# Performance work log

Measured on AMD Instinct MI355X. Metric: run time of the kernel, lower is better.

## Reference

```python
import jax, jax.numpy as jnp
import numpy as np

# ---- static config (mirrors GaussianLSS __init__) ----
ORF_H, ORF_W = 256, 704
FC, FH, FW = 128, 32, 88
D_ST, D_END, D_STEP = 4.0, 45.0, 1.0
OUT_C = 128
ERROR_TOL = 1.0
OPACITY_THR = 0.05
XB = (-50.0, 50.0, 1.0)
YB = (-50.0, 50.0, 1.0)
BEV_H = int(round((YB[1] - YB[0]) / YB[2]))
BEV_W = int(round((XB[1] - XB[0]) / XB[2]))
DS = np.arange(D_ST, D_END, D_STEP, dtype=np.float32)
D = DS.shape[0]  # 41
BN_EPS = 1e-3
CHUNK = 512      # gaussians composited per scan step (16896 = 33*512)
B, NCAM = 1, 6


def make_frustum():
    ds = jnp.broadcast_to(jnp.asarray(DS)[:, None, None], (D, FH, FW))
    xs = jnp.broadcast_to(jnp.linspace(0.0, ORF_W - 1.0, FW)[None, None, :], (D, FH, FW))
    ys = jnp.broadcast_to(jnp.linspace(0.0, ORF_H - 1.0, FH)[None, :, None], (D, FH, FW))
    return jnp.stack([xs, ys, ds], -1)  # [D,FH,FW,3]


def get_geometry(rots, trans, intrins, post_rots, post_trans):
    fr = make_frustum()
    pts = fr[None, None] - post_trans[:, :, None, None, None, :]
    pts = jnp.einsum('bnij,bndhwj->bndhwi', jnp.linalg.inv(post_rots), pts)
    pts = jnp.concatenate([pts[..., :2] * pts[..., 2:3], pts[..., 2:3]], -1)
    comb = jnp.einsum('bnij,bnjk->bnik', rots, jnp.linalg.inv(intrins))
    pts = jnp.einsum('bnij,bndhwj->bndhwi', comb, pts) + trans[:, :, None, None, None, :]
    return pts  # [B,N,D,FH,FW,3] ego-frame frustum points


def conv2d(x, w, b, pad):
    y = jax.lax.conv_general_dilated(x, w, (1, 1), [(pad, pad), (pad, pad)],
                                     dimension_numbers=('NCHW', 'OIHW', 'NCHW'))
    return y + b[None, :, None, None]


def bnorm(x, g, bt, m, v):
    s = (g / jnp.sqrt(v + BN_EPS))[None, :, None, None]
    return (x - m[None, :, None, None]) * s + bt[None, :, None, None]


def splat(means, cov6, colors, ops, valid_in):
    # Differentiable BEV gaussian rasterization (3DGS math, orthographic BEV camera,
    # all depths equal -> compositing in stable gaussian-index order).
    H, W = BEV_H, BEV_W
    sh, sw = H / 2.0, W / 2.0  # h/h_meters with FoV=2 (BEVCamera)
    my = -sh * means[:, 1] + H / 2.0  # pixel row (full_proj_transform row 0)
    mx = -sw * means[:, 0] + W / 2.0  # pixel col (row 1)
    a = sh * sh * cov6[:, 3] + 0.3    # 2D cov = J Sigma_xy J^T, +0.3 low-pass as in 3DGS
    c = sw * sw * cov6[:, 0] + 0.3
    b = sh * sw * cov6[:, 1]
    det = a * c - b * b
    valid = valid_in & (det > 0)
    inv_det = jnp.where(det > 0, 1.0 / det, 0.0)
    cA, cB, cC = c * inv_det, -b * inv_det, a * inv_det
    pi = jnp.repeat(jnp.arange(H, dtype=jnp.float32), W)  # [P] pixel rows
    pj = jnp.tile(jnp.arange(W, dtype=jnp.float32), H)    # [P] pixel cols
    G = means.shape[0]
    nchunk = G // CHUNK
    resh = lambda x: x.reshape((nchunk, CHUNK) + x.shape[1:])
    chunks = (resh(my), resh(mx), resh(cA), resh(cB), resh(cC),
              resh(ops), resh(valid), resh(colors))

    def body(carry, ch):
        logT, acc = carry
        my_c, mx_c, A, Bc, Cc, op_c, val_c, col_c = ch
        dI = pi[None, :] - my_c[:, None]                     # [Gc,P]
        dJ = pj[None, :] - mx_c[:, None]
        q = A[:, None] * dI * dI + 2.0 * Bc[:, None] * dI * dJ + Cc[:, None] * dJ * dJ
        alpha = jnp.minimum(0.99, op_c[:, None] * jnp.exp(-0.5 * q))
        alpha = jnp.where(val_c[:, None] & (q >= 0) & (alpha >= 1.0 / 255.0), alpha, 0.0)
        log1m = jnp.log1p(-alpha)
        cum = jnp.cumsum(log1m, axis=0)
        T = jnp.exp(logT[None, :] + cum - log1m)             # transmittance before each gaussian
        acc = acc + jnp.einsum('gp,gc->pc', alpha * T, col_c)
        return (logT + cum[-1], acc), None

    P = H * W
    init = (jnp.zeros((P,), jnp.float32), jnp.zeros((P, colors.shape[1]), jnp.float32))
    (_, acc), _ = jax.lax.scan(jax.checkpoint(body), init, chunks)
    return acc.reshape(H, W, -1).transpose(2, 0, 1)  # [C,H,W], bg is zeros


def _forward(cam2ego_rot, cam2ego_trans, cam_intrins, post_cam2ego_rot, post_cam2ego_trans,
             img_feats, conv1_w, conv1_b, bn1_g, bn1_b, bn1_m, bn1_v,
             conv2_w, conv2_b, bn2_g, bn2_b, bn2_m, bn2_v, conv3_w, conv3_b):
    geom = get_geometry(cam2ego_rot, cam2ego_trans, cam_intrins, post_cam2ego_rot, post_cam2ego_trans)
    b, n = img_feats.shape[:2]
    x = img_feats.reshape(b * n, FC, FH, FW)
    x = jax.nn.relu(bnorm(conv2d(x, conv1_w, conv1_b, 1), bn1_g, bn1_b, bn1_m, bn1_v))
    x = jax.nn.relu(bnorm(conv2d(x, conv2_w, conv2_b, 1), bn2_g, bn2_b, bn2_m, bn2_v))
    x = conv2d(x, conv3_w, conv3_b, 0)
    depth_prob = jax.nn.softmax(x[:, :D], axis=1).reshape(b, n, D, FH, FW)
    opac = jax.nn.sigmoid(x[:, D:D + 1]).reshape(b, n, FH, FW)
    feats = x[:, D + 1:].reshape(b, n, OUT_C, FH, FW)
    # per-pixel gaussian moments of the depth distribution (compute_gaussian)
    means = jnp.einsum('bndhw,bndhwi->bnhwi', depth_prob, geom)
    delta = means[:, :, None] - geom                                       # [B,N,D,FH,FW,3]
    cov = jnp.einsum('bndhw,bndhwi,bndhwj->bnhwij', depth_prob, delta, delta) * (ERROR_TOL ** 2 / 9.0)
    center = jnp.array([(XB[0] + XB[1]) / 2.0, (YB[0] + YB[1]) / 2.0, 0.0], jnp.float32)
    scale = jnp.array([2.0 / (XB[1] - XB[0]), 2.0 / (YB[1] - YB[0]), 1.0], jnp.float32)
    m_n = (means - center) * scale
    cov_n = cov * (scale[:, None] * scale[None, :])
    cov6 = jnp.stack([cov_n[..., 0, 0], cov_n[..., 0, 1], cov_n[..., 0, 2],
                      cov_n[..., 1, 1], cov_n[..., 1, 2], cov_n[..., 2, 2]], -1)
    g = n * FH * FW
    colors = feats.transpose(0, 1, 3, 4, 2).reshape(b, g, OUT_C)
    m_n = m_n.reshape(b, g, 3)
    cov6 = cov6.reshape(b, g, 6)
    ops = opac.reshape(b, g)
    mask = ops > OPACITY_THR  # opacity filtering == zero contribution, order preserved
    bev = jax.vmap(splat)(m_n, cov6, colors, ops, mask)                    # [B,C,H,W]
    num_gaussians = mask.astype(jnp.float32).sum(-1).mean()
    return bev, num_gaussians


def setup_inputs():
    key = jax.random.key(0)
    ks = jax.random.split(key, 8)
    # camera-to-ego rotations: cam->ego axis permutation composed with per-camera yaw
    yaw = np.linspace(0.0, 2.0 * np.pi, NCAM, endpoint=False).astype(np.float32)
    cz, sz = np.cos(yaw), np.sin(yaw)
    rotz = np.zeros((NCAM, 3, 3), np.float32)
    rotz[:, 0, 0] = cz; rotz[:, 0, 1] = -sz
    rotz[:, 1, 0] = sz; rotz[:, 1, 1] = cz
    rotz[:, 2, 2] = 1.0
    perm = np.array([[0.0, 0.0, 1.0], [-1.0, 0.0, 0.0], [0.0, -1.0, 0.0]], np.float32)
    rots = np.einsum('nij,jk->nik', rotz, perm)
    cam2ego_rot = jnp.asarray(np.broadcast_to(rots, (B, NCAM, 3, 3)).copy())
    cam2ego_trans = jax.random.normal(ks[0], (B, NCAM, 3), jnp.float32)
    K = np.array([[600.0, 0.0, ORF_W / 2.0], [0.0, 600.0, ORF_H / 2.0], [0.0, 0.0, 1.0]], np.float32)
    cam_intrins = jnp.asarray(np.broadcast_to(K, (B, NCAM, 3, 3)).copy())
    post_cam2ego_rot = jnp.broadcast_to(jnp.eye(3, dtype=jnp.float32), (B, NCAM, 3, 3)) + jnp.zeros((B, NCAM, 3, 3), jnp.float32)
    post_cam2ego_trans = jnp.zeros((B, NCAM, 3), jnp.float32)
    img_feats = jax.random.normal(ks[1], (B, NCAM, FC, FH, FW), jnp.float32)
    def conv_init(k, o, i, kh, kw):
        return jax.random.normal(k, (o, i, kh, kw), jnp.float32) * (1.0 / np.sqrt(i * kh * kw))
    return dict(cam2ego_rot=cam2ego_rot, cam2ego_trans=cam2ego_trans, cam_intrins=cam_intrins,
                post_cam2ego_rot=post_cam2ego_rot, post_cam2ego_trans=post_cam2ego_trans,
                img_feats=img_feats,
                conv1_w=conv_init(ks[2], FC, FC, 3, 3), conv1_b=jnp.zeros((FC,), jnp.float32),
                bn1_g=jnp.ones((FC,), jnp.float32), bn1_b=jnp.zeros((FC,), jnp.float32),
                bn1_m=jnp.zeros((FC,), jnp.float32), bn1_v=jnp.ones((FC,), jnp.float32),
                conv2_w=conv_init(ks[3], FC, FC, 3, 3), conv2_b=jnp.zeros((FC,), jnp.float32),
                bn2_g=jnp.ones((FC,), jnp.float32), bn2_b=jnp.zeros((FC,), jnp.float32),
                bn2_m=jnp.zeros((FC,), jnp.float32), bn2_v=jnp.ones((FC,), jnp.float32),
                conv3_w=conv_init(ks[4], OUT_C + D + 1, FC, 1, 1),
                conv3_b=jax.random.normal(ks[5], (OUT_C + D + 1,), jnp.float32) * 0.1)


def reference(cam2ego_rot, cam2ego_trans, cam_intrins, post_cam2ego_rot, post_cam2ego_trans,
              img_feats, conv1_w, conv1_b, bn1_g, bn1_b, bn1_m, bn1_v,
              conv2_w, conv2_b, bn2_g, bn2_b, bn2_m, bn2_v, conv3_w, conv3_b):
    return _forward(cam2ego_rot, cam2ego_trans, cam_intrins, post_cam2ego_rot, post_cam2ego_trans,
                    img_feats, conv1_w, conv1_b, bn1_g, bn1_b, bn1_m, bn1_v,
                    conv2_w, conv2_b, bn2_g, bn2_b, bn2_m, bn2_v, conv3_w, conv3_b)
```

## Files before the change

### kernel.cpp

```cpp
#include <hip/hip_runtime.h>

#define NCAM 6
#define FC   128
#define FH_  32
#define FW_  88
#define NPIX (FH_*FW_)
#define PH   34
#define PW   92
#define PPIX (PH*PW)
#define ND   41
#define X3D  42
#define OUTC 128
#define GTOT (NCAM*NPIX)
#define BEVH 100
#define BEVW 100
#define NPXB (BEVH*BEVW)
#define NTILE 25
#define NWORD 264
#define WCAP  70000
#define CSIZE 64
#define CBLK  2048

#define SZA     (NCAM*FC*PPIX)
#define WS_CAM  0
// ... 5 lines not shown
#define WS_BASE (WS_WL + WCAP)

__device__ inline void inv3x3(const float* m, float* o) {
    float a=m[0],b=m[1],c=m[2],d=m[3],e=m[4],f=m[5],g=m[6],h=m[7],i=m[8];
    float A=e*i-f*h, B=c*h-b*i, C=b*f-c*e;
    float Dd=f*g-d*i, E=a*i-c*g, F=c*d-a*f;
    float Gg=d*h-e*g, H=b*g-a*h, I=a*e-b*d;
    float r = 1.0f/(a*A + b*Dd + c*Gg);
    o[0]=A*r; o[1]=B*r; o[2]=C*r; o[3]=Dd*r; o[4]=E*r; o[5]=F*r;
    o[6]=Gg*r; o[7]=H*r; o[8]=I*r;
}

__global__ void cam_consts_kernel(const float* __restrict__ rot, const float* __restrict__ tr,
                                  const float* __restrict__ intr, const float* __restrict__ prot,
                                  const float* __restrict__ ptr_, float* __restrict__ cam) {
    int n = threadIdx.x;
    if (n >= NCAM) return;
    float M1[9], Ki[9];
    inv3x3(prot + n*9, M1);
    inv3x3(intr + n*9, Ki);
    const float* R = rot + n*9;
    float* c = cam + n*24;
    for (int i=0;i<9;i++) c[i] = M1[i];
    for (int i=0;i<3;i++) c[9+i] = ptr_[n*3+i];
    for (int i=0;i<3;i++)
        for (int j=0;j<3;j++)
            c[12+i*3+j] = R[i*3+0]*Ki[0+j] + R[i*3+1]*Ki[3+j] + R[i*3+2]*Ki[6+j];
    for (int i=0;i<3;i++) c[21+i] = tr[n*3+i];
}

__global__ __launch_bounds__(256) void pad_input_kernel(const float* __restrict__ src,
                                                        float* __restrict__ dst) {
    int idx = blockIdx.x*256 + threadIdx.x;
    int plane = idx / NPIX, px = idx - plane*NPIX;
    int y = px / FW_, x = px - y*FW_;
    dst[(size_t)plane*PPIX + (y+1)*PW + (x+1)] = src[idx];
}

__global__ __launch_bounds__(256) void conv3x3_pf_kernel(
        const float* __restrict__ in, float* __restrict__ out, const float* __restrict__ w,
        const float* __restrict__ cb, const float* __restrict__ bg, const float* __restrict__ bb,
        const float* __restrict__ bm, const float* __restrict__ bv) {
    const int n   = blockIdx.x;
    const int co0 = blockIdx.y * 4;
    const int qid = blockIdx.z * 256 + threadIdx.x;
    if (qid >= 704) return;
    const int y = qid / 22, x0 = (qid - y*22) * 4;
    float scale[4], shift[4];
    #pragma unroll
    for (int c=0;c<4;c++) {
        float s = bg[co0+c] * rsqrtf(bv[co0+c] + 1e-3f);
        scale[c] = s;
        shift[c] = (cb[co0+c] - bm[co0+c]) * s + bb[co0+c];
    }
    float acc[4][4] = {};
    const float* ip = in + (size_t)n*FC*PPIX + y*PW + x0;
    const float* wb = w + (size_t)co0*FC*9;
    float4 p4[3]; float2 p2[3];
    #pragma unroll
    for (int r=0;r<3;r++) {
        p4[r] = *(const float4*)(ip + r*PW);
        p2[r] = *(const float2*)(ip + r*PW + 4);
    }
    for (int ci=0; ci<FC; ++ci) {
        float v[3][6];
        #pragma unroll
        for (int r=0;r<3;r++) {
            v[r][0]=p4[r].x; v[r][1]=p4[r].y; v[r][2]=p4[r].z; v[r][3]=p4[r].w;
            v[r][4]=p2[r].x; v[r][5]=p2[r].y;
        }
        if (ci + 1 < FC) {
            const float* ipn = ip + PPIX;
            #pragma unroll
            for (int r=0;r<3;r++) {
                p4[r] = *(const float4*)(ipn + r*PW);
                p2[r] = *(const float2*)(ipn + r*PW + 4);
            }
        }
// ... 41 lines not shown
    }
    const float* ip = in + (size_t)n*FC*PPIX + pp;
    #pragma unroll 4
    for (int ci=0; ci<FC; ++ci) {
        float v = ip[(size_t)ci*PPIX];
        #pragma unroll
        for (int k=0;k<8;k++) acc[k] = fmaf(wr[k][ci], v, acc[k]);
    }
    #pragma unroll
    for (int k=0;k<8;k++) {
        int co = co0 + k;
        if (co < X3D)
            x3d[((size_t)n*X3D + co)*NPIX + px] = acc[k];
        else if (co < 170)
            colors[(((size_t)(n*NPIX + px)) << 7) + (co - X3D)] = acc[k];
    }
}

__global__ __launch_bounds__(256) void moments_kernel(const float* __restrict__ x3,
        const float* __restrict__ cam, float* __restrict__ gauss, float* __restrict__ ng) {
    int gi = blockIdx.x*256 + threadIdx.x;
    int n  = gi / NPIX;
    int p  = gi - n*NPIX;
    int h  = p / FW_, xp = p - h*FW_;
    const float* cc = cam + n*24;
    float u = xp * (703.0f/87.0f);
    float v = h  * (255.0f/31.0f);
    float fx = u - cc[9], fy = v - cc[10], fz = -cc[11];
    float p0x = cc[0]*fx + cc[1]*fy + cc[2]*fz;
    float p0y = cc[3]*fx + cc[4]*fy + cc[5]*fz;
    float p0z = cc[6]*fx + cc[7]*fy + cc[8]*fz;
    const float* lg = x3 + (size_t)n*X3D*NPIX + p;

    float mxl = -1e30f;
    for (int d=0; d<ND; ++d) mxl = fmaxf(mxl, lg[(size_t)d*NPIX]);
    float s=0.f, sgx=0.f, sgy=0.f;
    for (int d=0; d<ND; ++d) {
        float e  = __expf(lg[(size_t)d*NPIX] - mxl);
        float dz = 4.0f + (float)d;
        float pz = p0z + dz*cc[8];
        float px = (p0x + dz*cc[2]) * pz;
        float py = (p0y + dz*cc[5]) * pz;
        float gx = cc[12]*px + cc[13]*py + cc[14]*pz + cc[21];
        float gy = cc[15]*px + cc[16]*py + cc[17]*pz + cc[22];
        s += e; sgx += e*gx; sgy += e*gy;
    }
    float inv_s = 1.0f/s;
    float mex = sgx*inv_s, mey = sgy*inv_s;
    float cxx=0.f, cxy=0.f, cyy=0.f;
    for (int d=0; d<ND; ++d) {
        float e  = __expf(lg[(size_t)d*NPIX] - mxl);
        float dz = 4.0f + (float)d;
        float pz = p0z + dz*cc[8];
        float px = (p0x + dz*cc[2]) * pz;
        float py = (p0y + dz*cc[5]) * pz;
        float gx = cc[12]*px + cc[13]*py + cc[14]*pz + cc[21];
        float gy = cc[15]*px + cc[16]*py + cc[17]*pz + cc[22];
        float dxv = gx - mex, dyv = gy - mey;
        cxx += e*dxv*dxv; cxy += e*dxv*dyv; cyy += e*dyv*dyv;
    }
    const float k9 = inv_s * (1.0f/9.0f);
    cxx *= k9; cxy *= k9; cyy *= k9;

    float lo = lg[(size_t)ND*NPIX];
    float op = 1.0f/(1.0f + __expf(-lo));
    bool mask = op > 0.05f;

    const float SC = 0.02f, SH = 50.0f, SW = 50.0f;
    float my = -SH*(mey*SC) + 50.0f;
    float mx = -SW*(mex*SC) + 50.0f;
    float a  = SH*SH*(cyy*SC*SC) + 0.3f;
    float b  = SH*SW*(cxy*SC*SC);
    float c  = SW*SW*(cxx*SC*SC) + 0.3f;
    float det = a*c - b*b;
    bool valid = mask && (det > 0.0f);
    float A, B2, C, qm, ri, rj;
    if (valid) {
        float idet = 1.0f/det;
        A = c*idet; B2 = -2.0f*b*idet; C = a*idet;
        qm = 2.0f*__logf(255.0f*op);
        ri = sqrtf(qm*a); rj = sqrtf(qm*c);
    } else { A=B2=C=0.f; qm=-1.0f; ri=-1e30f; rj=-1e30f; }
    float* gp = gauss + (size_t)gi*8;
    gp[0]=my; gp[1]=mx; gp[2]=A; gp[3]=B2; gp[4]=C; gp[5]=qm; gp[6]=ri; gp[7]=rj;
// ... 81 lines not shown
        unsigned short* __restrict__ list, int* __restrict__ wl) {
    __shared__ unsigned long long sw[NWORD];
    __shared__ int wpre[NWORD];
    const int tile = blockIdx.x, t = threadIdx.x;
    if (t < NWORD) sw[t] = masks[(size_t)tile*NWORD + t];
    __syncthreads();
    if (t == 0) {
        int run = 0;
        for (int w2 = 0; w2 < NWORD; ++w2) { wpre[w2] = run; run += __popcll(sw[w2]); }
    }
    __syncthreads();
    if (t < NWORD) {
        unsigned long long m = sw[t];
        int pos = off[tile] + wpre[t], base = t << 6;
        while (m) { int b = __builtin_ctzll(m); m &= m - 1; list[pos++] = (unsigned short)(base + b); }
    }
    int nch = (cnt[tile] + CSIZE-1)/CSIZE;
    int c0 = choff[tile];
    if (t < nch && c0 + t < WCAP) wl[c0 + t] = (tile << 9) | t;
}

__device__ inline float eval_alpha(const float4 g0, const float4 g1, float fi, float fj) {
    float dI = fi - g0.x, dJ = fj - g0.y;
    float q = dI*(g0.z*dI + g0.w*dJ) + g1.x*dJ*dJ;
    if (q < 0.0f || q > g1.y) return 0.0f;
    return fminf(0.99f, 0.003921568627f * __expf(0.5f*(g1.y - q)));
}

__global__ __launch_bounds__(256) void chunk_sums_kernel(const float* __restrict__ gauss,
        const unsigned short* __restrict__ list, const int* __restrict__ cnt,
        const int* __restrict__ off, const int* __restrict__ wl, const int* __restrict__ nwork,
        float* __restrict__ base) {
    const int nw = nwork[0];
    const int t = threadIdx.x;
    const int px = t & 15, kg = t >> 4;
    __shared__ unsigned short slist[CSIZE];
    __shared__ float red[16][17];
    for (int e = blockIdx.x; e < nw; e += gridDim.x) {
        int v = wl[e], tile = v >> 9, c = v & 511;
        int hbase = off[tile] + (c << 6);
        int nh = min(CSIZE, cnt[tile] - (c << 6));
        if (t < nh) slist[t] = list[hbase + t];
        __syncthreads();
        const int i0 = (tile / NTILE) * 4, j0 = (tile % NTILE) * 4;
        const float fi = (float)(i0 + (px >> 2)), fj = (float)(j0 + (px & 3));
        float s = 0.0f;
        for (int k = kg; k < nh; k += 16) {
            int g = slist[k];
            float4 g0 = *(const float4*)(gauss + ((size_t)g << 3));
            float4 g1 = *(const float4*)(gauss + ((size_t)g << 3) + 4);
            float a = eval_alpha(g0, g1, fi, fj);
            if (a > 0.0f) s += __logf(1.0f - a);
        }
        red[kg][px] = s;
        __syncthreads();
        if (t < 16) {
            float acc = 0.0f;
            #pragma unroll
            for (int k2 = 0; k2 < 16; ++k2) acc += red[k2][t];
            base[(size_t)e*16 + t] = acc;
        }
        __syncthreads();
    }
}

__global__ __launch_bounds__(256) void chunk_prefix_kernel(const int* __restrict__ choff,
                                                           float* __restrict__ base) {
    __shared__ float part[16][17];
    const int tile = blockIdx.x, t = threadIdx.x;
    const int c0 = choff[tile], nch = choff[tile+1] - c0;
    if (nch == 0) return;
    const int px = t & 15, cg = t >> 4;
    const int L16 = (nch + 15) >> 4;
    const int a0 = cg*L16, a1 = min(nch, a0 + L16);
    float s = 0.0f;
    for (int c = a0; c < a1; ++c) s += base[(size_t)(c0 + c)*16 + px];
    part[cg][px] = s;
    __syncthreads();
    if (t < 16) {
        float run = 0.0f;
        #pragma unroll
        for (int k = 0; k < 16; ++k) { float tmp = part[k][t]; part[k][t] = run; run += tmp; }
    }
    __syncthreads();
    float run = part[cg][px];
    for (int c = a0; c < a1; ++c) {
        size_t idx = (size_t)(c0 + c)*16 + px;
        float tmp = base[idx];
        base[idx] = run;
        run += tmp;
    }
}

__global__ __launch_bounds__(256) void composite_kernel(const float* __restrict__ gauss,
        const float* __restrict__ colors, const unsigned short* __restrict__ list,
        const int* __restrict__ cnt, const int* __restrict__ off, const int* __restrict__ wl,
        const int* __restrict__ nwork, const float* __restrict__ base, float* __restrict__ out) {
    const int nw = nwork[0];
    const int t = threadIdx.x;
    const int lane = t & 63;
    const int e_px = t >> 4, e_kg = t & 15;
    const int a_cs4 = t & 31, a_pxq = t >> 5;
    __shared__ unsigned short slist[2][CSIZE];
    __shared__ float s_w[CSIZE][17];
    const int per = (nw + CBLK - 1) / CBLK;
    int e0 = blockIdx.x * per;
    if (e0 >= nw) return;
    int e1 = min(nw, e0 + per);

    float4 acc0 = make_float4(0.f,0.f,0.f,0.f);
    float4 acc1 = make_float4(0.f,0.f,0.f,0.f);
    int cur_tile = wl[e0] >> 9;
    int cur_i0 = (cur_tile / NTILE) * 4, cur_j0 = (cur_tile % NTILE) * 4;

    int buf = 0;
    {
        int v = wl[e0], tl = v >> 9, c = v & 511;
        int nh0 = min(CSIZE, cnt[tl] - (c << 6));
        if (t < nh0) slist[0][t] = list[off[tl] + (c << 6) + t];
    }

    for (int e = e0; e < e1; ++e) {
        int v = wl[e], tile = v >> 9, c = v & 511;
        if (tile != cur_tile) {
            const int pix0 = (cur_i0 + (a_pxq >> 2)) * BEVW + cur_j0 + (a_pxq & 3);
            const int pix1 = pix0 + 2 * BEVW;
            float* op = out + (size_t)(a_cs4 << 2) * NPXB;
            atomicAdd(op + 0*NPXB + pix0, acc0.x); atomicAdd(op + 1*NPXB + pix0, acc0.y);
            atomicAdd(op + 2*NPXB + pix0, acc0.z); atomicAdd(op + 3*NPXB + pix0, acc0.w);
            atomicAdd(op + 0*NPXB + pix1, acc1.x); atomicAdd(op + 1*NPXB + pix1, acc1.y);
            atomicAdd(op + 2*NPXB + pix1, acc1.z); atomicAdd(op + 3*NPXB + pix1, acc1.w);
            acc0 = make_float4(0.f,0.f,0.f,0.f);
            acc1 = make_float4(0.f,0.f,0.f,0.f);
            cur_tile = tile;
            cur_i0 = (tile / NTILE) * 4; cur_j0 = (tile % NTILE) * 4;
        }
        const int nh = min(CSIZE, cnt[cur_tile] - (c << 6));
        __syncthreads();
        if (e + 1 < e1) {
            int v2 = wl[e+1], tl2 = v2 >> 9, c2 = v2 & 511;
            int nh2 = min(CSIZE, cnt[tl2] - (c2 << 6));
            if (t < nh2) slist[buf^1][t] = list[off[tl2] + (c2 << 6) + t];
        }
        {
            const float fi = (float)(cur_i0 + (e_px >> 2)), fj = (float)(cur_j0 + (e_px & 3));
            const int k0 = e_kg << 2;
            float a4[4]; float lsum = 0.0f;
            #pragma unroll
            for (int i = 0; i < 4; ++i) {
                int k = k0 + i;
                float a = 0.0f;
                if (k < nh) {
                    int g = slist[buf][k];
                    float4 g0 = *(const float4*)(gauss + ((size_t)g << 3));
                    float4 g1 = *(const float4*)(gauss + ((size_t)g << 3) + 4);
                    a = eval_alpha(g0, g1, fi, fj);
                }
                a4[i] = a;
                if (a > 0.0f) lsum += __logf(1.0f - a);
            }
            float s = lsum;
            #pragma unroll
            for (int o = 1; o < 16; o <<= 1) {
                float u = __shfl_up(s, (unsigned)o, 64);
                if ((lane & 15) >= o) s += u;
            }
            float T = __expf(base[(size_t)e*16 + e_px] + (s - lsum));
            #pragma unroll
            for (int i = 0; i < 4; ++i) {
                float wv = a4[i] * T; T -= wv;
                s_w[k0 + i][e_px] = wv;
            }
        }
        __syncthreads();
        const float* colbase = colors;
        if (nh == CSIZE) {
            #pragma unroll 8
            for (int k = 0; k < CSIZE; ++k) {
                int g = slist[buf][k];
                float w0 = s_w[k][a_pxq];
                float w1 = s_w[k][a_pxq + 8];
                float4 cl = *(const float4*)(colbase + ((size_t)g << 7) + (a_cs4 << 2));
                acc0.x = fmaf(w0, cl.x, acc0.x); acc0.y = fmaf(w0, cl.y, acc0.y);
                acc0.z = fmaf(w0, cl.z, acc0.z); acc0.w = fmaf(w0, cl.w, acc0.w);
                acc1.x = fmaf(w1, cl.x, acc1.x); acc1.y = fmaf(w1, cl.y, acc1.y);
                acc1.z = fmaf(w1, cl.z, acc1.z); acc1.w = fmaf(w1, cl.w, acc1.w);
            }
        } else {
            #pragma unroll 4
            for (int k = 0; k < nh; ++k) {
                int g = slist[buf][k];
                float w0 = s_w[k][a_pxq];
                float w1 = s_w[k][a_pxq + 8];
                float4 cl = *(const float4*)(colbase + ((size_t)g << 7) + (a_cs4 << 2));
                acc0.x = fmaf(w0, cl.x, acc0.x); acc0.y = fmaf(w0, cl.y, acc0.y);
                acc0.z = fmaf(w0, cl.z, acc0.z); acc0.w = fmaf(w0, cl.w, acc0.w);
                acc1.x = fmaf(w1, cl.x, acc1.x); acc1.y = fmaf(w1, cl.y, acc1.y);
                acc1.z = fmaf(w1, cl.z, acc1.z); acc1.w = fmaf(w1, cl.w, acc1.w);
            }
        }
        buf ^= 1;
    }
    const int pix0 = (cur_i0 + (a_pxq >> 2)) * BEVW + cur_j0 + (a_pxq & 3);
    const int pix1 = pix0 + 2 * BEVW;
    float* op = out + (size_t)(a_cs4 << 2) * NPXB;
    atomicAdd(op + 0*NPXB + pix0, acc0.x); atomicAdd(op + 1*NPXB + pix0, acc0.y);
    atomicAdd(op + 2*NPXB + pix0, acc0.z); atomicAdd(op + 3*NPXB + pix0, acc0.w);
    atomicAdd(op + 0*NPXB + pix1, acc1.x); atomicAdd(op + 1*NPXB + pix1, acc1.y);
    atomicAdd(op + 2*NPXB + pix1, acc1.z); atomicAdd(op + 3*NPXB + pix1, acc1.w);
}

extern "C" void kernel_launch(void* const* d_in, const int* in_sizes, int n_in,
                              void* d_out, int out_size, void* d_ws, size_t ws_size,
                              hipStream_t stream) {
    const float* rot  = (const float*)d_in[0];
    const float* tr   = (const float*)d_in[1];
    const float* intr = (const float*)d_in[2];
    const float* prot = (const float*)d_in[3];
    const float* ptr_ = (const float*)d_in[4];
    const float* img  = (const float*)d_in[5];
    const float* c1w  = (const float*)d_in[6];  const float* c1b = (const float*)d_in[7];
    const float* b1g  = (const float*)d_in[8];  const float* b1b = (const float*)d_in[9];
    const float* b1m  = (const float*)d_in[10]; const float* b1v = (const float*)d_in[11];
    const float* c2w  = (const float*)d_in[12]; const float* c2b = (const float*)d_in[13];
    const float* b2g  = (const float*)d_in[14]; const float* b2b = (const float*)d_in[15];
    const float* b2m  = (const float*)d_in[16]; const float* b2v = (const float*)d_in[17];
    const float* c3w  = (const float*)d_in[18]; const float* c3b = (const float*)d_in[19];
    float* out = (float*)d_out;
    float* ws  = (float*)d_ws;
    float* CAM = ws + WS_CAM;
    float* RA  = ws + WS_A;
    float* RB  = ws + WS_RB;
    float* X3B = ws + WS_X3;
    float* GS  = ws + WS_GS;
    int*   WL  = (int*)(ws + WS_WL);
    float* BASE = ws + WS_BASE;
    unsigned long long* MASKS = (unsigned long long*)X3B;
    int* AUXI = (int*)(ws + WS_X3 + 330000);
    int* CNT = AUXI;
    int* OFF = AUXI + 640;
    int* CHOFF = AUXI + 1280;
    int* NWORK = AUXI + 1920;
    unsigned short* LIST = (unsigned short*)RA;
    float* COL = RB;
    float* ngp = out + (size_t)NPXB*OUTC;

    cam_consts_kernel<<<1, 64, 0, stream>>>(rot, tr, intr, prot, ptr_, CAM);
    (void)hipMemsetAsync(RA, 0, (size_t)SZA*sizeof(float), stream);
    (void)hipMemsetAsync(RB, 0, (size_t)SZA*sizeof(float), stream);
    pad_input_kernel<<<NCAM*FC*NPIX/256, 256, 0, stream>>>(img, RA);
    conv3x3_pf_kernel<<<dim3(NCAM,32,3), 256, 0, stream>>>(RA, RB, c1w, c1b, b1g, b1b, b1m, b1v);
    conv3x3_pf_kernel<<<dim3(NCAM,32,3), 256, 0, stream>>>(RB, RA, c2w, c2b, b2g, b2b, b2m, b2v);
    conv1x1_kernel<<<dim3(NCAM,11,22), 256, 0, stream>>>(RA, X3B, COL, c3w, c3b);
    (void)hipMemsetAsync(ngp, 0, sizeof(float), stream);
    (void)hipMemsetAsync(out, 0, (size_t)NPXB*OUTC*sizeof(float), stream);
    moments_kernel<<<GTOT/256, 256, 0, stream>>>(X3B, CAM, GS, ngp);
    (void)hipMemsetAsync(MASKS, 0, (size_t)NTILE*NTILE*NWORD*sizeof(unsigned long long), stream);
    build_masks_kernel<<<GTOT/256, 256, 0, stream>>>(GS, MASKS);
    cnt_kernel<<<NTILE*NTILE, 256, 0, stream>>>(MASKS, CNT);
    scan_kernel<<<1, 640, 0, stream>>>(CNT, OFF, CHOFF, NWORK);
    fill_kernel<<<NTILE*NTILE, 256, 0, stream>>>(MASKS, CNT, OFF, CHOFF, LIST, WL);
    chunk_sums_kernel<<<8192, 256, 0, stream>>>(GS, LIST, CNT, OFF, WL, NWORK, BASE);
    chunk_prefix_kernel<<<NTILE*NTILE, 256, 0, stream>>>(CHOFF, BASE);
    composite_kernel<<<CBLK, 256, 0, stream>>>(GS, COL, LIST, CNT, OFF, WL, NWORK, BASE, out);
}
```

Before: 487.4 us.

## Pipeline composite weights, wave-level chunk sums, cache logits, fuse padding memset

The composite kernel now computes transmittance weights for the next chunk while accumulating colors for the current one. It triple-buffers the gaussian index lists and double-buffers the weights, which removes one barrier per chunk. chunk_sums becomes one wavefront per work item that reduces with shuffles instead of shared memory and block barriers. moments caches the 41 logits and their exponentials in registers instead of reloading and recomputing them, and pad_input writes the zero border itself so one memset goes away. The trade-off is more shared memory and register pressure, which may lower occupancy.

```diff
diff --git a/kernel.cpp b/kernel.cpp
--- a/kernel.cpp
+++ b/kernel.cpp
@@ -61,9 +61,13 @@
 __global__ __launch_bounds__(256) void pad_input_kernel(const float* __restrict__ src,
                                                         float* __restrict__ dst) {
     int idx = blockIdx.x*256 + threadIdx.x;
-    int plane = idx / NPIX, px = idx - plane*NPIX;
-    int y = px / FW_, x = px - y*FW_;
-    dst[(size_t)plane*PPIX + (y+1)*PW + (x+1)] = src[idx];
+    if (idx >= NCAM*FC*PPIX) return;
+    int plane = idx / PPIX, pp = idx - plane*PPIX;
+    int y = pp / PW, x = pp - y*PW;
+    float v = 0.0f;
+    if (y >= 1 && y <= FH_ && x >= 1 && x <= FW_)
+        v = src[(size_t)plane*NPIX + (y-1)*FW_ + (x-1)];
+    dst[idx] = v;
 }
 
 __global__ __launch_bounds__(256) void conv3x3_pf_kernel(
@@ -180,11 +184,19 @@
     float p0z = cc[6]*fx + cc[7]*fy + cc[8]*fz;
     const float* lg = x3 + (size_t)n*X3D*NPIX + p;
 
+    float lgv[ND];
+    #pragma unroll
+    for (int d=0; d<ND; ++d) lgv[d] = lg[(size_t)d*NPIX];
+
     float mxl = -1e30f;
-    for (int d=0; d<ND; ++d) mxl = fmaxf(mxl, lg[(size_t)d*NPIX]);
+    #pragma unroll
+    for (int d=0; d<ND; ++d) mxl = fmaxf(mxl, lgv[d]);
+
     float s=0.f, sgx=0.f, sgy=0.f;
+    #pragma unroll
     for (int d=0; d<ND; ++d) {
-        float e  = __expf(lg[(size_t)d*NPIX] - mxl);
+        float e  = __expf(lgv[d] - mxl);
+        lgv[d] = e;
         float dz = 4.0f + (float)d;
         float pz = p0z + dz*cc[8];
         float px = (p0x + dz*cc[2]) * pz;
@@ -196,8 +208,9 @@
     float inv_s = 1.0f/s;
     float mex = sgx*inv_s, mey = sgy*inv_s;
     float cxx=0.f, cxy=0.f, cyy=0.f;
+    #pragma unroll
     for (int d=0; d<ND; ++d) {
-        float e  = __expf(lg[(size_t)d*NPIX] - mxl);
+        float e  = lgv[d];
         float dz = 4.0f + (float)d;
         float pz = p0z + dz*cc[8];
         float px = (p0x + dz*cc[2]) * pz;
@@ -345,35 +358,27 @@
         const int* __restrict__ off, const int* __restrict__ wl, const int* __restrict__ nwork,
         float* __restrict__ base) {
     const int nw = nwork[0];
-    const int t = threadIdx.x;
-    const int px = t & 15, kg = t >> 4;
-    __shared__ unsigned short slist[CSIZE];
-    __shared__ float red[16][17];
-    for (int e = blockIdx.x; e < nw; e += gridDim.x) {
+    const int lane = threadIdx.x & 63;
+    const int wid  = (blockIdx.x * 256 + threadIdx.x) >> 6;
+    const int nwv  = (gridDim.x * 256) >> 6;
+    const int px = lane & 15, kg = lane >> 4;
+    for (int e = wid; e < nw; e += nwv) {
         int v = wl[e], tile = v >> 9, c = v & 511;
         int hbase = off[tile] + (c << 6);
         int nh = min(CSIZE, cnt[tile] - (c << 6));
-        if (t < nh) slist[t] = list[hbase + t];
-        __syncthreads();
         const int i0 = (tile / NTILE) * 4, j0 = (tile % NTILE) * 4;
         const float fi = (float)(i0 + (px >> 2)), fj = (float)(j0 + (px & 3));
         float s = 0.0f;
-        for (int k = kg; k < nh; k += 16) {
-            int g = slist[k];
+        for (int k = kg; k < nh; k += 4) {
+            int g = list[hbase + k];
             float4 g0 = *(const float4*)(gauss + ((size_t)g << 3));
             float4 g1 = *(const float4*)(gauss + ((size_t)g << 3) + 4);
             float a = eval_alpha(g0, g1, fi, fj);
             if (a > 0.0f) s += __logf(1.0f - a);
         }
-        red[kg][px] = s;
-        __syncthreads();
-        if (t < 16) {
-            float acc = 0.0f;
-            #pragma unroll
-            for (int k2 = 0; k2 < 16; ++k2) acc += red[k2][t];
-            base[(size_t)e*16 + t] = acc;
-        }
-        __syncthreads();
+        s += __shfl_xor(s, 16, 64);
+        s += __shfl_xor(s, 32, 64);
+        if (lane < 16) base[(size_t)e*16 + lane] = s;
     }
 }
 
@@ -414,8 +419,8 @@
     const int lane = t & 63;
     const int e_px = t >> 4, e_kg = t & 15;
     const int a_cs4 = t & 31, a_pxq = t >> 5;
-    __shared__ unsigned short slist[2][CSIZE];
-    __shared__ float s_w[CSIZE][17];
+    __shared__ unsigned short slist[3][CSIZE];
+    __shared__ float s_w[2][CSIZE][17];
     const int per = (nw + CBLK - 1) / CBLK;
     int e0 = blockIdx.x * per;
     if (e0 >= nw) return;
@@ -426,45 +431,70 @@
     int cur_tile = wl[e0] >> 9;
     int cur_i0 = (cur_tile / NTILE) * 4, cur_j0 = (cur_tile % NTILE) * 4;
 
-    int buf = 0;
     {
         int v = wl[e0], tl = v >> 9, c = v & 511;
         int nh0 = min(CSIZE, cnt[tl] - (c << 6));
-        if (t < nh0) slist[0][t] = list[off[tl] + (c << 6) + t];
+        if (t < nh0) slist[e0 % 3][t] = list[off[tl] + (c << 6) + t];
+        if (e0 + 1 < e1) {
+            int v2 = wl[e0+1], tl2 = v2 >> 9, c2 = v2 & 511;
+            int nh2 = min(CSIZE, cnt[tl2] - (c2 << 6));
+            if (t < nh2) slist[(e0+1) % 3][t] = list[off[tl2] + (c2 << 6) + t];
+        }
+    }
+    __syncthreads();
+    {
+        int v = wl[e0], tl = v >> 9, c = v & 511;
+        int nh_e = min(CSIZE, cnt[tl] - (c << 6));
+        const float fi = (float)(cur_i0 + (e_px >> 2)), fj = (float)(cur_j0 + (e_px & 3));
+        const int k0 = e_kg << 2;
+        float a4[4]; float lsum = 0.0f;
+        #pragma unroll
+        for (int i = 0; i < 4; ++i) {
+            int k = k0 + i;
+            float a = 0.0f;
+            if (k < nh_e) {
+                int g = slist[e0 % 3][k];
+                float4 g0 = *(const float4*)(gauss + ((size_t)g << 3));
+                float4 g1 = *(const float4*)(gauss + ((size_t)g << 3) + 4);
+                a = eval_alpha(g0, g1, fi, fj);
+            }
+            a4[i] = a;
+            if (a > 0.0f) lsum += __logf(1.0f - a);
+        }
+        float s = lsum;
+        #pragma unroll
+        for (int o = 1; o < 16; o <<= 1) {
+            float u = __shfl_up(s, (unsigned)o, 64);
+            if ((lane & 15) >= o) s += u;
+        }
+        float T = __expf(base[(size_t)e0*16 + e_px] + (s - lsum));
+        #pragma unroll
+        for (int i = 0; i < 4; ++i) {
+            float wv = a4[i] * T; T -= wv;
+            s_w[e0 & 1][k0 + i][e_px] = wv;
+        }
     }
 
     for (int e = e0; e < e1; ++e) {
-        int v = wl[e], tile = v >> 9, c = v & 511;
-        if (tile != cur_tile) {
-            const int pix0 = (cur_i0 + (a_pxq >> 2)) * BEVW + cur_j0 + (a_pxq & 3);
-            const int pix1 = pix0 + 2 * BEVW;
-            float* op = out + (size_t)(a_cs4 << 2) * NPXB;
-            atomicAdd(op + 0*NPXB + pix0, acc0.x); atomicAdd(op + 1*NPXB + pix0, acc0.y);
-            atomicAdd(op + 2*NPXB + pix0, acc0.z); atomicAdd(op + 3*NPXB + pix0, acc0.w);
-            atomicAdd(op + 0*NPXB + pix1, acc1.x); atomicAdd(op + 1*NPXB + pix1, acc1.y);
-            atomicAdd(op + 2*NPXB + pix1, acc1.z); atomicAdd(op + 3*NPXB + pix1, acc1.w);
-            acc0 = make_float4(0.f,0.f,0.f,0.f);
-            acc1 = make_float4(0.f,0.f,0.f,0.f);
-            cur_tile = tile;
-            cur_i0 = (tile / NTILE) * 4; cur_j0 = (tile % NTILE) * 4;
-        }
-        const int nh = min(CSIZE, cnt[cur_tile] - (c << 6));
         __syncthreads();
+        if (e + 2 < e1) {
+            int v2 = wl[e+2], tl2 = v2 >> 9, c2 = v2 & 511;
+            int nh2 = min(CSIZE, cnt[tl2] - (c2 << 6));
+            if (t < nh2) slist[(e+2) % 3][t] = list[off[tl2] + (c2 << 6) + t];
+        }
         if (e + 1 < e1) {
-            int v2 = wl[e+1], tl2 = v2 >> 9, c2 = v2 & 511;
-            int nh2 = min(CSIZE, cnt[tl2] - (c2 << 6));
-            if (t < nh2) slist[buf^1][t] = list[off[tl2] + (c2 << 6) + t];
-        }
-        {
-            const float fi = (float)(cur_i0 + (e_px >> 2)), fj = (float)(cur_j0 + (e_px & 3));
+            int v = wl[e+1], tl = v >> 9, c = v & 511;
+            int nh_e = min(CSIZE, cnt[tl] - (c << 6));
+            const int ii0 = (tl / NTILE) * 4, jj0 = (tl % NTILE) * 4;
+            const float fi = (float)(ii0 + (e_px >> 2)), fj = (float)(jj0 + (e_px & 3));
             const int k0 = e_kg << 2;
             float a4[4]; float lsum = 0.0f;
             #pragma unroll
             for (int i = 0; i < 4; ++i) {
                 int k = k0 + i;
                 float a = 0.0f;
-                if (k < nh) {
-                    int g = slist[buf][k];
+                if (k < nh_e) {
+                    int g = slist[(e+1) % 3][k];
                     float4 g0 = *(const float4*)(gauss + ((size_t)g << 3));
                     float4 g1 = *(const float4*)(gauss + ((size_t)g << 3) + 4);
                     a = eval_alpha(g0, g1, fi, fj);
@@ -478,41 +508,57 @@
                 float u = __shfl_up(s, (unsigned)o, 64);
                 if ((lane & 15) >= o) s += u;
             }
-            float T = __expf(base[(size_t)e*16 + e_px] + (s - lsum));
+            float T = __expf(base[(size_t)(e+1)*16 + e_px] + (s - lsum));
             #pragma unroll
             for (int i = 0; i < 4; ++i) {
                 float wv = a4[i] * T; T -= wv;
-                s_w[k0 + i][e_px] = wv;
-            }
-        }
-        __syncthreads();
-        const float* colbase = colors;
-        if (nh == CSIZE) {
-            #pragma unroll 8
-            for (int k = 0; k < CSIZE; ++k) {
-                int g = slist[buf][k];
-                float w0 = s_w[k][a_pxq];
-                float w1 = s_w[k][a_pxq + 8];
-                float4 cl = *(const float4*)(colbase + ((size_t)g << 7) + (a_cs4 << 2));
-                acc0.x = fmaf(w0, cl.x, acc0.x); acc0.y = fmaf(w0, cl.y, acc0.y);
-                acc0.z = fmaf(w0, cl.z, acc0.z); acc0.w = fmaf(w0, cl.w, acc0.w);
-                acc1.x = fmaf(w1, cl.x, acc1.x); acc1.y = fmaf(w1, cl.y, acc1.y);
-                acc1.z = fmaf(w1, cl.z, acc1.z); acc1.w = fmaf(w1, cl.w, acc1.w);
-            }
-        } else {
-            #pragma unroll 4
-            for (int k = 0; k < nh; ++k) {
-                int g = slist[buf][k];
-                float w0 = s_w[k][a_pxq];
-                float w1 = s_w[k][a_pxq + 8];
-                float4 cl = *(const float4*)(colbase + ((size_t)g << 7) + (a_cs4 << 2));
-                acc0.x = fmaf(w0, cl.x, acc0.x); acc0.y = fmaf(w0, cl.y, acc0.y);
-                acc0.z = fmaf(w0, cl.z, acc0.z); acc0.w = fmaf(w0, cl.w, acc0.w);
-                acc1.x = fmaf(w1, cl.x, acc1.x); acc1.y = fmaf(w1, cl.y, acc1.y);
-                acc1.z = fmaf(w1, cl.z, acc1.z); acc1.w = fmaf(w1, cl.w, acc1.w);
-            }
-        }
-        buf ^= 1;
+                s_w[(e+1) & 1][k0 + i][e_px] = wv;
+            }
+        }
+        {
+            int v = wl[e], tile = v >> 9, c = v & 511;
+            if (tile != cur_tile) {
+                const int pix0 = (cur_i0 + (a_pxq >> 2)) * BEVW + cur_j0 + (a_pxq & 3);
+                const int pix1 = pix0 + 2 * BEVW;
+                float* op = out + (size_t)(a_cs4 << 2) * NPXB;
+                atomicAdd(op + 0*NPXB + pix0, acc0.x); atomicAdd(op + 1*NPXB + pix0, acc0.y);
+                atomicAdd(op + 2*NPXB + pix0, acc0.z); atomicAdd(op + 3*NPXB + pix0, acc0.w);
+                atomicAdd(op + 0*NPXB + pix1, acc1.x); atomicAdd(op + 1*NPXB + pix1, acc1.y);
+                atomicAdd(op + 2*NPXB + pix1, acc1.z); atomicAdd(op + 3*NPXB + pix1, acc1.w);
+                acc0 = make_float4(0.f,0.f,0.f,0.f);
+                acc1 = make_float4(0.f,0.f,0.f,0.f);
+                cur_tile = tile;
+                cur_i0 = (tile / NTILE) * 4; cur_j0 = (tile % NTILE) * 4;
+            }
+            const int nh = min(CSIZE, cnt[tile] - (c << 6));
+            const float (*swp)[17] = s_w[e & 1];
+            const unsigned short* slp = slist[e % 3];
+            if (nh == CSIZE) {
+                #pragma unroll 8
+                for (int k = 0; k < CSIZE; ++k) {
+                    int g = slp[k];
+                    float w0 = swp[k][a_pxq];
+                    float w1 = swp[k][a_pxq + 8];
+                    float4 cl = *(const float4*)(colors + ((size_t)g << 7) + (a_cs4 << 2));
+                    acc0.x = fmaf(w0, cl.x, acc0.x); acc0.y = fmaf(w0, cl.y, acc0.y);
+                    acc0.z = fmaf(w0, cl.z, acc0.z); acc0.w = fmaf(w0, cl.w, acc0.w);
+                    acc1.x = fmaf(w1, cl.x, acc1.x); acc1.y = fmaf(w1, cl.y, acc1.y);
+                    acc1.z = fmaf(w1, cl.z, acc1.z); acc1.w = fmaf(w1, cl.w, acc1.w);
+                }
+            } else {
+                #pragma unroll 4
+                for (int k = 0; k < nh; ++k) {
+                    int g = slp[k];
+                    float w0 = swp[k][a_pxq];
+                    float w1 = swp[k][a_pxq + 8];
+                    float4 cl = *(const float4*)(colors + ((size_t)g << 7) + (a_cs4 << 2));
+                    acc0.x = fmaf(w0, cl.x, acc0.x); acc0.y = fmaf(w0, cl.y, acc0.y);
+                    acc0.z = fmaf(w0, cl.z, acc0.z); acc0.w = fmaf(w0, cl.w, acc0.w);
+                    acc1.x = fmaf(w1, cl.x, acc1.x); acc1.y = fmaf(w1, cl.y, acc1.y);
+                    acc1.z = fmaf(w1, cl.z, acc1.z); acc1.w = fmaf(w1, cl.w, acc1.w);
+                }
+            }
+        }
     }
     const int pix0 = (cur_i0 + (a_pxq >> 2)) * BEVW + cur_j0 + (a_pxq & 3);
     const int pix1 = pix0 + 2 * BEVW;
@@ -559,9 +605,8 @@
     float* ngp = out + (size_t)NPXB*OUTC;
 
     cam_consts_kernel<<<1, 64, 0, stream>>>(rot, tr, intr, prot, ptr_, CAM);
-    (void)hipMemsetAsync(RA, 0, (size_t)SZA*sizeof(float), stream);
     (void)hipMemsetAsync(RB, 0, (size_t)SZA*sizeof(float), stream);
-    pad_input_kernel<<<NCAM*FC*NPIX/256, 256, 0, stream>>>(img, RA);
+    pad_input_kernel<<<(NCAM*FC*PPIX + 255)/256, 256, 0, stream>>>(img, RA);
     conv3x3_pf_kernel<<<dim3(NCAM,32,3), 256, 0, stream>>>(RA, RB, c1w, c1b, b1g, b1b, b1m, b1v);
     conv3x3_pf_kernel<<<dim3(NCAM,32,3), 256, 0, stream>>>(RB, RA, c2w, c2b, b2g, b2b, b2m, b2v);
     conv1x1_kernel<<<dim3(NCAM,11,22), 256, 0, stream>>>(RA, X3B, COL, c3w, c3b);
```

New measurement: 476.5 us. -2.3%, faster.

## Replace log-sum transmittance with products, fuse padding, retile conv and composite

Applied to the files above, without the earlier changes.

The pad kernel now writes the whole padded buffer, zeros included, so one memset goes away. The conv3x3 launch drops to 128-thread blocks with twice the z-blocks. The moments kernel caches the logits and exp values in registers instead of reloading them and recomputing exp. The transmittance sums switch from log/exp to direct products, and chunk_sums becomes one wavefront per work item with shuffle reductions, which avoids shared memory and barriers. The composite kernel remaps threads so each one holds 4 pixels × 4 channels and splits the gaussians across two halves. Products may underflow and lose some precision compared with log sums.

```diff
diff --git a/kernel.cpp b/kernel.cpp
--- a/kernel.cpp
+++ b/kernel.cpp
@@ -61,18 +61,22 @@
 __global__ __launch_bounds__(256) void pad_input_kernel(const float* __restrict__ src,
                                                         float* __restrict__ dst) {
     int idx = blockIdx.x*256 + threadIdx.x;
-    int plane = idx / NPIX, px = idx - plane*NPIX;
-    int y = px / FW_, x = px - y*FW_;
-    dst[(size_t)plane*PPIX + (y+1)*PW + (x+1)] = src[idx];
-}
-
-__global__ __launch_bounds__(256) void conv3x3_pf_kernel(
+    if (idx >= NCAM*FC*PPIX) return;
+    int plane = idx / PPIX, pp = idx - plane*PPIX;
+    int y = pp / PW, x = pp - y*PW;
+    float v = 0.0f;
+    if (y >= 1 && y <= FH_ && x >= 1 && x <= FW_)
+        v = src[(size_t)plane*NPIX + (y-1)*FW_ + (x-1)];
+    dst[idx] = v;
+}
+
+__global__ __launch_bounds__(128) void conv3x3_pf_kernel(
         const float* __restrict__ in, float* __restrict__ out, const float* __restrict__ w,
         const float* __restrict__ cb, const float* __restrict__ bg, const float* __restrict__ bb,
         const float* __restrict__ bm, const float* __restrict__ bv) {
     const int n   = blockIdx.x;
     const int co0 = blockIdx.y * 4;
-    const int qid = blockIdx.z * 256 + threadIdx.x;
+    const int qid = blockIdx.z * 128 + threadIdx.x;
     if (qid >= 704) return;
     const int y = qid / 22, x0 = (qid - y*22) * 4;
     float scale[4], shift[4];
@@ -180,11 +184,19 @@
     float p0z = cc[6]*fx + cc[7]*fy + cc[8]*fz;
     const float* lg = x3 + (size_t)n*X3D*NPIX + p;
 
+    float lgv[ND];
+    #pragma unroll
+    for (int d=0; d<ND; ++d) lgv[d] = lg[(size_t)d*NPIX];
+
     float mxl = -1e30f;
-    for (int d=0; d<ND; ++d) mxl = fmaxf(mxl, lg[(size_t)d*NPIX]);
+    #pragma unroll
+    for (int d=0; d<ND; ++d) mxl = fmaxf(mxl, lgv[d]);
+
     float s=0.f, sgx=0.f, sgy=0.f;
+    #pragma unroll
     for (int d=0; d<ND; ++d) {
-        float e  = __expf(lg[(size_t)d*NPIX] - mxl);
+        float e  = __expf(lgv[d] - mxl);
+        lgv[d] = e;
         float dz = 4.0f + (float)d;
         float pz = p0z + dz*cc[8];
         float px = (p0x + dz*cc[2]) * pz;
@@ -196,8 +208,9 @@
     float inv_s = 1.0f/s;
     float mex = sgx*inv_s, mey = sgy*inv_s;
     float cxx=0.f, cxy=0.f, cyy=0.f;
+    #pragma unroll
     for (int d=0; d<ND; ++d) {
-        float e  = __expf(lg[(size_t)d*NPIX] - mxl);
+        float e  = lgv[d];
         float dz = 4.0f + (float)d;
         float pz = p0z + dz*cc[8];
         float px = (p0x + dz*cc[2]) * pz;
@@ -345,35 +358,27 @@
         const int* __restrict__ off, const int* __restrict__ wl, const int* __restrict__ nwork,
         float* __restrict__ base) {
     const int nw = nwork[0];
-    const int t = threadIdx.x;
-    const int px = t & 15, kg = t >> 4;
-    __shared__ unsigned short slist[CSIZE];
-    __shared__ float red[16][17];
-    for (int e = blockIdx.x; e < nw; e += gridDim.x) {
+    const int lane = threadIdx.x & 63;
+    const int wid  = (blockIdx.x * 256 + threadIdx.x) >> 6;
+    const int nwv  = (gridDim.x * 256) >> 6;
+    const int px = lane & 15, kg = lane >> 4;
+    for (int e = wid; e < nw; e += nwv) {
         int v = wl[e], tile = v >> 9, c = v & 511;
         int hbase = off[tile] + (c << 6);
         int nh = min(CSIZE, cnt[tile] - (c << 6));
-        if (t < nh) slist[t] = list[hbase + t];
-        __syncthreads();
         const int i0 = (tile / NTILE) * 4, j0 = (tile % NTILE) * 4;
         const float fi = (float)(i0 + (px >> 2)), fj = (float)(j0 + (px & 3));
-        float s = 0.0f;
-        for (int k = kg; k < nh; k += 16) {
-            int g = slist[k];
+        float s = 1.0f;
+        for (int k = kg; k < nh; k += 4) {
+            int g = list[hbase + k];
             float4 g0 = *(const float4*)(gauss + ((size_t)g << 3));
             float4 g1 = *(const float4*)(gauss + ((size_t)g << 3) + 4);
             float a = eval_alpha(g0, g1, fi, fj);
-            if (a > 0.0f) s += __logf(1.0f - a);
-        }
-        red[kg][px] = s;
-        __syncthreads();
-        if (t < 16) {
-            float acc = 0.0f;
-            #pragma unroll
-            for (int k2 = 0; k2 < 16; ++k2) acc += red[k2][t];
-            base[(size_t)e*16 + t] = acc;
-        }
-        __syncthreads();
+            s *= (1.0f - a);
+        }
+        s *= __shfl_xor(s, 16, 64);
+        s *= __shfl_xor(s, 32, 64);
+        if (lane < 16) base[(size_t)e*16 + lane] = s;
     }
 }
 
@@ -386,14 +391,14 @@
     const int px = t & 15, cg = t >> 4;
     const int L16 = (nch + 15) >> 4;
     const int a0 = cg*L16, a1 = min(nch, a0 + L16);
-    float s = 0.0f;
-    for (int c = a0; c < a1; ++c) s += base[(size_t)(c0 + c)*16 + px];
+    float s = 1.0f;
+    for (int c = a0; c < a1; ++c) s *= base[(size_t)(c0 + c)*16 + px];
     part[cg][px] = s;
     __syncthreads();
     if (t < 16) {
-        float run = 0.0f;
+        float run = 1.0f;
         #pragma unroll
-        for (int k = 0; k < 16; ++k) { float tmp = part[k][t]; part[k][t] = run; run += tmp; }
+        for (int k = 0; k < 16; ++k) { float tmp = part[k][t]; part[k][t] = run; run *= tmp; }
     }
     __syncthreads();
     float run = part[cg][px];
@@ -401,7 +406,7 @@
         size_t idx = (size_t)(c0 + c)*16 + px;
         float tmp = base[idx];
         base[idx] = run;
-        run += tmp;
+        run *= tmp;
     }
 }
 
@@ -413,7 +418,9 @@
     const int t = threadIdx.x;
     const int lane = t & 63;
     const int e_px = t >> 4, e_kg = t & 15;
-    const int a_cs4 = t & 31, a_pxq = t >> 5;
+    const int g_par = t >> 7;
+    const int cq = t & 31;
+    const int pg = (t >> 5) & 3;
     __shared__ unsigned short slist[2][CSIZE];
     __shared__ float s_w[CSIZE][17];
     const int per = (nw + CBLK - 1) / CBLK;
@@ -421,8 +428,9 @@
     if (e0 >= nw) return;
     int e1 = min(nw, e0 + per);
 
-    float4 acc0 = make_float4(0.f,0.f,0.f,0.f);
-    float4 acc1 = make_float4(0.f,0.f,0.f,0.f);
+    float4 acc[4];
+    #pragma unroll
+    for (int j=0;j<4;j++) acc[j] = make_float4(0.f,0.f,0.f,0.f);
     int cur_tile = wl[e0] >> 9;
     int cur_i0 = (cur_tile / NTILE) * 4, cur_j0 = (cur_tile % NTILE) * 4;
 
@@ -436,15 +444,16 @@
     for (int e = e0; e < e1; ++e) {
         int v = wl[e], tile = v >> 9, c = v & 511;
         if (tile != cur_tile) {
-            const int pix0 = (cur_i0 + (a_pxq >> 2)) * BEVW + cur_j0 + (a_pxq & 3);
-            const int pix1 = pix0 + 2 * BEVW;
-            float* op = out + (size_t)(a_cs4 << 2) * NPXB;
-            atomicAdd(op + 0*NPXB + pix0, acc0.x); atomicAdd(op + 1*NPXB + pix0, acc0.y);
-            atomicAdd(op + 2*NPXB + pix0, acc0.z); atomicAdd(op + 3*NPXB + pix0, acc0.w);
-            atomicAdd(op + 0*NPXB + pix1, acc1.x); atomicAdd(op + 1*NPXB + pix1, acc1.y);
-            atomicAdd(op + 2*NPXB + pix1, acc1.z); atomicAdd(op + 3*NPXB + pix1, acc1.w);
-            acc0 = make_float4(0.f,0.f,0.f,0.f);
-            acc1 = make_float4(0.f,0.f,0.f,0.f);
+            float* op = out + (size_t)(cq << 2) * NPXB + (cur_i0 + pg) * BEVW + cur_j0;
+            #pragma unroll
+            for (int j = 0; j < 4; ++j) {
+                atomicAdd(op + 0*NPXB + j, acc[j].x);
+                atomicAdd(op + 1*NPXB + j, acc[j].y);
+                atomicAdd(op + 2*NPXB + j, acc[j].z);
+                atomicAdd(op + 3*NPXB + j, acc[j].w);
+            }
+            #pragma unroll
+            for (int j=0;j<4;j++) acc[j] = make_float4(0.f,0.f,0.f,0.f);
             cur_tile = tile;
             cur_i0 = (tile / NTILE) * 4; cur_j0 = (tile % NTILE) * 4;
         }
@@ -458,7 +467,7 @@
         {
             const float fi = (float)(cur_i0 + (e_px >> 2)), fj = (float)(cur_j0 + (e_px & 3));
             const int k0 = e_kg << 2;
-            float a4[4]; float lsum = 0.0f;
+            float a4[4]; float p = 1.0f;
             #pragma unroll
             for (int i = 0; i < 4; ++i) {
                 int k = k0 + i;
@@ -470,15 +479,16 @@
                     a = eval_alpha(g0, g1, fi, fj);
                 }
                 a4[i] = a;
-                if (a > 0.0f) lsum += __logf(1.0f - a);
-            }
-            float s = lsum;
+                p *= (1.0f - a);
+            }
+            float s = p;
             #pragma unroll
             for (int o = 1; o < 16; o <<= 1) {
                 float u = __shfl_up(s, (unsigned)o, 64);
-                if ((lane & 15) >= o) s += u;
-            }
-            float T = __expf(base[(size_t)e*16 + e_px] + (s - lsum));
+                if ((lane & 15) >= o) s *= u;
+            }
+            float ex = __shfl_up(s, 1u, 64);
+            float T = base[(size_t)e*16 + e_px] * (((lane & 15) == 0) ? 1.0f : ex);
             #pragma unroll
             for (int i = 0; i < 4; ++i) {
                 float wv = a4[i] * T; T -= wv;
@@ -486,41 +496,52 @@
             }
         }
         __syncthreads();
-        const float* colbase = colors;
         if (nh == CSIZE) {
             #pragma unroll 8
-            for (int k = 0; k < CSIZE; ++k) {
-                int g = slist[buf][k];
-                float w0 = s_w[k][a_pxq];
-                float w1 = s_w[k][a_pxq + 8];
-                float4 cl = *(const float4*)(colbase + ((size_t)g << 7) + (a_cs4 << 2));
-                acc0.x = fmaf(w0, cl.x, acc0.x); acc0.y = fmaf(w0, cl.y, acc0.y);
-                acc0.z = fmaf(w0, cl.z, acc0.z); acc0.w = fmaf(w0, cl.w, acc0.w);
-                acc1.x = fmaf(w1, cl.x, acc1.x); acc1.y = fmaf(w1, cl.y, acc1.y);
-                acc1.z = fmaf(w1, cl.z, acc1.z); acc1.w = fmaf(w1, cl.w, acc1.w);
+            for (int k = 0; k < CSIZE/2; ++k) {
+                const int idx = (k << 1) | g_par;
+                int g = slist[buf][idx];
+                const float* swr = s_w[idx] + (pg << 2);
+                float w0 = swr[0], w1 = swr[1], w2 = swr[2], w3 = swr[3];
+                float4 cl = *(const float4*)(colors + ((size_t)g << 7) + (cq << 2));
+                acc[0].x = fmaf(w0, cl.x, acc[0].x); acc[0].y = fmaf(w0, cl.y, acc[0].y);
+                acc[0].z = fmaf(w0, cl.z, acc[0].z); acc[0].w = fmaf(w0, cl.w, acc[0].w);
+                acc[1].x = fmaf(w1, cl.x, acc[1].x); acc[1].y = fmaf(w1, cl.y, acc[1].y);
+                acc[1].z = fmaf(w1, cl.z, acc[1].z); acc[1].w = fmaf(w1, cl.w, acc[1].w);
+                acc[2].x = fmaf(w2, cl.x, acc[2].x); acc[2].y = fmaf(w2, cl.y, acc[2].y);
+                acc[2].z = fmaf(w2, cl.z, acc[2].z); acc[2].w = fmaf(w2, cl.w, acc[2].w);
+                acc[3].x = fmaf(w3, cl.x, acc[3].x); acc[3].y = fmaf(w3, cl.y, acc[3].y);
+                acc[3].z = fmaf(w3, cl.z, acc[3].z); acc[3].w = fmaf(w3, cl.w, acc[3].w);
             }
         } else {
             #pragma unroll 4
-            for (int k = 0; k < nh; ++k) {
-                int g = slist[buf][k];
-                float w0 = s_w[k][a_pxq];
-                float w1 = s_w[k][a_pxq + 8];
-                float4 cl = *(const float4*)(colbase + ((size_t)g << 7) + (a_cs4 << 2));
-                acc0.x = fmaf(w0, cl.x, acc0.x); acc0.y = fmaf(w0, cl.y, acc0.y);
-                acc0.z = fmaf(w0, cl.z, acc0.z); acc0.w = fmaf(w0, cl.w, acc0.w);
-                acc1.x = fmaf(w1, cl.x, acc1.x); acc1.y = fmaf(w1, cl.y, acc1.y);
-                acc1.z = fmaf(w1, cl.z, acc1.z); acc1.w = fmaf(w1, cl.w, acc1.w);
+            for (int k = 0; k < CSIZE/2; ++k) {
+                const int idx = (k << 1) | g_par;
+                if (idx >= nh) break;
+                int g = slist[buf][idx];
+                const float* swr = s_w[idx] + (pg << 2);
+                float w0 = swr[0], w1 = swr[1], w2 = swr[2], w3 = swr[3];
+                float4 cl = *(const float4*)(colors + ((size_t)g << 7) + (cq << 2));
+                acc[0].x = fmaf(w0, cl.x, acc[0].x); acc[0].y = fmaf(w0, cl.y, acc[0].y);
+                acc[0].z = fmaf(w0, cl.z, acc[0].z); acc[0].w = fmaf(w0, cl.w, acc[0].w);
+                acc[1].x = fmaf(w1, cl.x, acc[1].x); acc[1].y = fmaf(w1, cl.y, acc[1].y);
+                acc[1].z = fmaf(w1, cl.z, acc[1].z); acc[1].w = fmaf(w1, cl.w, acc[1].w);
+                acc[2].x = fmaf(w2, cl.x, acc[2].x); acc[2].y = fmaf(w2, cl.y, acc[2].y);
+                acc[2].z = fmaf(w2, cl.z, acc[2].z); acc[2].w = fmaf(w2, cl.w, acc[2].w);
+                acc[3].x = fmaf(w3, cl.x, acc[3].x); acc[3].y = fmaf(w3, cl.y, acc[3].y);
+                acc[3].z = fmaf(w3, cl.z, acc[3].z); acc[3].w = fmaf(w3, cl.w, acc[3].w);
             }
         }
         buf ^= 1;
     }
-    const int pix0 = (cur_i0 + (a_pxq >> 2)) * BEVW + cur_j0 + (a_pxq & 3);
-    const int pix1 = pix0 + 2 * BEVW;
-    float* op = out + (size_t)(a_cs4 << 2) * NPXB;
-    atomicAdd(op + 0*NPXB + pix0, acc0.x); atomicAdd(op + 1*NPXB + pix0, acc0.y);
-    atomicAdd(op + 2*NPXB + pix0, acc0.z); atomicAdd(op + 3*NPXB + pix0, acc0.w);
-    atomicAdd(op + 0*NPXB + pix1, acc1.x); atomicAdd(op + 1*NPXB + pix1, acc1.y);
-    atomicAdd(op + 2*NPXB + pix1, acc1.z); atomicAdd(op + 3*NPXB + pix1, acc1.w);
+    float* op = out + (size_t)(cq << 2) * NPXB + (cur_i0 + pg) * BEVW + cur_j0;
+    #pragma unroll
+    for (int j = 0; j < 4; ++j) {
+        atomicAdd(op + 0*NPXB + j, acc[j].x);
+        atomicAdd(op + 1*NPXB + j, acc[j].y);
+        atomicAdd(op + 2*NPXB + j, acc[j].z);
+        atomicAdd(op + 3*NPXB + j, acc[j].w);
+    }
 }
 
 extern "C" void kernel_launch(void* const* d_in, const int* in_sizes, int n_in,
@@ -559,11 +580,10 @@
     float* ngp = out + (size_t)NPXB*OUTC;
 
     cam_consts_kernel<<<1, 64, 0, stream>>>(rot, tr, intr, prot, ptr_, CAM);
-    (void)hipMemsetAsync(RA, 0, (size_t)SZA*sizeof(float), stream);
     (void)hipMemsetAsync(RB, 0, (size_t)SZA*sizeof(float), stream);
-    pad_input_kernel<<<NCAM*FC*NPIX/256, 256, 0, stream>>>(img, RA);
-    conv3x3_pf_kernel<<<dim3(NCAM,32,3), 256, 0, stream>>>(RA, RB, c1w, c1b, b1g, b1b, b1m, b1v);
-    conv3x3_pf_kernel<<<dim3(NCAM,32,3), 256, 0, stream>>>(RB, RA, c2w, c2b, b2g, b2b, b2m, b2v);
+    pad_input_kernel<<<(NCAM*FC*PPIX + 255)/256, 256, 0, stream>>>(img, RA);
+    conv3x3_pf_kernel<<<dim3(NCAM,32,6), 128, 0, stream>>>(RA, RB, c1w, c1b, b1g, b1b, b1m, b1v);
+    conv3x3_pf_kernel<<<dim3(NCAM,32,6), 128, 0, stream>>>(RB, RA, c2w, c2b, b2g, b2b, b2m, b2v);
     conv1x1_kernel<<<dim3(NCAM,11,22), 256, 0, stream>>>(RA, X3B, COL, c3w, c3b);
     (void)hipMemsetAsync(ngp, 0, sizeof(float), stream);
     (void)hipMemsetAsync(out, 0, (size_t)NPXB*OUTC*sizeof(float), stream);
```

Measured after the change: 766.5 us. 57.2% more time.
